# Kernel optimization log

Hardware: AMD Instinct MI355X
Metric: run time of the kernel (lower is better)

The kernel has to match this reference:

```python
import jax, jax.numpy as jnp
import numpy as np

N_QUBITS = 12
LAYERS = 8
N_CLASS = 10
BATCH = 2048
FEAT = 3072  # CIFAR-10 flattened 3*32*32
DIM = 2 ** N_QUBITS


def _apply_ry_layer(psi, angles):
    """Apply Ry(angles[q]) to qubit q for all q. psi: [B, 2,...,2] complex.
    kron order in the torch code makes qubit 0 the MSB -> tensor axis q+1."""
    c, s = jnp.cos(angles), jnp.sin(angles)
    for q in range(N_QUBITS):
        rot = jnp.stack([jnp.stack([c[q], -s[q]]), jnp.stack([s[q], c[q]])]).astype(psi.dtype)
        # contract qubit axis with rot (rows index output): psi'[..a..] = rot[a,b] psi[..b..]
        psi = jnp.moveaxis(jnp.tensordot(psi, rot, axes=([q + 1], [1])), -1, q + 1)
    return psi


def _cnot(psi, control, target):
    """CNOT == proj0(c) x I(t) + proj1(c) x X(t): flip target bit where control bit is 1."""
    ca, ta = control + 1, target + 1
    flipped = jnp.flip(psi, axis=ta)          # X on target qubit
    p0 = jax.lax.index_in_dim(psi, 0, axis=ca, keepdims=True)      # control = 0: identity
    p1 = jax.lax.index_in_dim(flipped, 1, axis=ca, keepdims=True)  # control = 1: X
    return jnp.concatenate([p0, p1], axis=ca)


def setup_inputs() -> dict:
    key = jax.random.key(0)
    kx, ka, kw = jax.random.split(key, 3)
    x = jax.random.normal(kx, (BATCH, FEAT), dtype=jnp.float32)
    angles = jax.random.uniform(ka, (LAYERS, N_QUBITS), minval=-0.01, maxval=0.01, dtype=jnp.float32)
    W = jax.random.normal(kw, (N_CLASS, DIM), dtype=jnp.float32) * np.float32(1.0 / np.sqrt(DIM))
    b = jnp.zeros((N_CLASS,), dtype=jnp.float32)
    return {"x": x, "angles": angles, "W": W, "b": b}


def reference(x, angles, W, b):
    B = x.shape[0]
    # CIFAR branch: right-pad features to 2^n, flatten (no-op for 2D), L2-normalize rows
    x = jnp.pad(x, ((0, 0), (0, DIM - x.shape[1])))
    x = x / jnp.linalg.norm(x, axis=1, keepdims=True)
    psi = x.astype(jnp.complex64).reshape((B,) + (2,) * N_QUBITS)
    for l in range(LAYERS):
        psi = _apply_ry_layer(psi, angles[l])
        # cx_linear_layer: CNOT(n-2,n-1), then CNOT(i,i+1) for i = n-3..0
        psi = _cnot(psi, N_QUBITS - 2, N_QUBITS - 1)
        for i in range(N_QUBITS - 3, -1, -1):
            psi = _cnot(psi, i, i + 1)
    probs = (psi.real ** 2 + psi.imag ** 2).reshape(B, DIM)  # Re(conj(psi)*psi)
    return probs @ W.T + b
```

## Files before the change

### kernel.cpp

```cpp
#include <hip/hip_runtime.h>
#include <math.h>

#define LAYERS  8
#define FEAT    3072
#define NCLASS  10
#define DIM     4096
#define ST      68

typedef float v2f __attribute__((ext_vector_type(2)));
typedef float v4f __attribute__((ext_vector_type(4)));

__device__ __forceinline__ int px6c(int r) {
    int u = r ^ (r >> 1); u ^= u >> 2; u ^= u >> 4; return u & 63;
}
__device__ __forceinline__ int gray6(int r) { return (r ^ (r >> 1)) & 63; }

__device__ __forceinline__ float getc(const v2f v[32], int u) {
    return (u & 1) ? v[u >> 1].y : v[u >> 1].x;
}
__device__ __forceinline__ void setc(v2f v[32], int u, float x) {
    if (u & 1) v[u >> 1].y = x; else v[u >> 1].x = x;
}
__device__ __forceinline__ float bpermf(int addr, float x) {
    return __int_as_float(__builtin_amdgcn_ds_bpermute(addr, __float_as_int(x)));
}

__device__ __forceinline__ void butterflies6(v2f v[32],
                                             const float* __restrict__ cl,
                                             const float* __restrict__ sl,
                                             int off) {
    {
        const float c = cl[off], s = sl[off];
        const v2f c2 = {c, c};
        const v2f ms = {-s, s};
#pragma unroll
        for (int i = 0; i < 32; ++i) {
            v2f a = v[i];
            v2f sw = {a.y, a.x};
            v[i] = a * c2 + sw * ms;
        }
    }
#pragma unroll
    for (int p = 1; p < 6; ++p) {
        const float c = cl[off - p], s = sl[off - p];
        const v2f c2 = {c, c};
        const v2f s2 = {s, s};
#pragma unroll
        for (int i0 = 0; i0 < 32; ++i0) {
            if (i0 & (1 << (p - 1))) continue;
            const int i1 = i0 | (1 << (p - 1));
            v2f a = v[i0], e = v[i1];
            v[i0] = a * c2 - e * s2;
            v[i1] = a * s2 + e * c2;
        }
    }
}

__device__ __forceinline__ void butterflies6_renamed(v2f v[32],
                                                     const float* __restrict__ cl,
                                                     const float* __restrict__ sl,
                                                     float psgn) {
    {
        const float c = cl[11], s = sl[11];
        const v2f c2 = {c, c};
        const v2f msA = {-s, s};
        const v2f msB = {s, -s};
#pragma unroll
        for (int k = 0; k < 32; ++k) {
            v2f a = v[k];
            v2f sw = {a.y, a.x};
            v[k] = a * c2 + sw * ((k & 1) ? msB : msA);
        }
    }
#pragma unroll
    for (int b = 1; b < 5; ++b) {
        const float c = cl[11 - b], s = sl[11 - b];
        const v2f c2 = {c, c};
#pragma unroll
        for (int m = 0; m < 32; ++m) {
            if (m & (1 << (b - 1))) continue;
            const int part = m ^ ((1 << b) - 1);
            const float sg = (m & (1 << b)) ? -s : s;
            const v2f sg2 = {sg, sg};
            const v2f A = v[m], E = v[part];
            const v2f Esw = {E.y, E.x};
            const v2f Asw = {A.y, A.x};
            v[m]    = A * c2 - Esw * sg2;
            v[part] = Asw * sg2 + E * c2;
        }
    }
    {
        const float c = cl[6];
        const float snl = psgn * sl[6];
        const v2f c2 = {c, c};
        const v2f sg2 = {snl, snl};
#pragma unroll
        for (int m = 0; m < 16; ++m) {
            const int part = m ^ 31;
            const v2f A = v[m], E = v[part];
            const v2f Esw = {E.y, E.x};
            const v2f Asw = {A.y, A.x};
            v[m]    = A * c2 - Esw * sg2;
            v[part] = Asw * sg2 + E * c2;
        }
    }
}

__global__ __launch_bounds__(64)
void qnn_kernel(const float* __restrict__ x,
                const float* __restrict__ ang,
                const float* __restrict__ W,
                const float* __restrict__ bias,
                float* __restrict__ out)
{
    __shared__ __attribute__((aligned(16))) float lds[ST * 64];
    __shared__ float cst[96], snt[96];

    const int t = threadIdx.x;
    const int b = blockIdx.x;

    {
        float a0 = ang[t];
        cst[t] = cosf(a0);
        snt[t] = sinf(a0);
        if (t < 32) {
            float a1 = ang[64 + t];
            cst[64 + t] = cosf(a1);
            snt[64 + t] = sinf(a1);
        }
    }

    v2f v[32];
    {
        const float* xb = x + (size_t)b * FEAT;
#pragma unroll
        for (int r = 0; r < 64; ++r) {
            if (r < FEAT / 64) setc(v, r, xb[64 * r + t]);
            else               setc(v, r, 0.f);
        }
    }

    float invn2;
    {
        v2f s2 = {0.f, 0.f};
#pragma unroll
        for (int i = 0; i < 32; ++i) s2 += v[i] * v[i];
        float ss = s2.x + s2.y;
#pragma unroll
        for (int o = 1; o < 64; o <<= 1) ss += __shfl_xor(ss, o, 64);
        invn2 = 1.0f / ss;
    }

    {
        const int slot = __builtin_amdgcn_s_getreg(4 | (0 << 6) | (3 << 11)) & 7;
#pragma unroll 1
        for (int i = 0; i < slot; ++i) __builtin_amdgcn_s_sleep(12);
    }

    int px = t ^ (t >> 1); px ^= px >> 2; px ^= px >> 4; px &= 63;
    const int A0 = 4 * px;
    const int A1 = 4 * (px ^ 63);
    const int u0 = t & 1;
    const float psgn = u0 ? -1.f : 1.f;
    const int gtl = gray6(t);
    const int bp  = gtl + 32 * ST * u0;
    const int bm  = gtl - 32 * ST * u0;

    {
        const float* cl = cst;
        const float* sl = snt;
        butterflies6(v, cl, sl, 5);
#pragma unroll
        for (int i = 0; i < 16; ++i) {
            v4f q = {v[2 * i].x, v[2 * i].y, v[2 * i + 1].x, v[2 * i + 1].y};
            *(v4f*)(lds + ST * t + 4 * i) = q;
        }
#pragma unroll
        for (int u = 0; u < 64; ++u)
            setc(v, u, lds[t + ST * u]);
        butterflies6(v, cl, sl, 11);
    }

#pragma unroll 1
    for (int p = 0; p < 4; ++p) {
        {
            const float* cl = cst + (2 * p + 1) * 12;
            const float* sl = snt + (2 * p + 1) * 12;

            butterflies6_renamed(v, cl, sl, psgn);

#pragma unroll
            for (int s = 0; s < 64; ++s) {
                const int g = gray6(s);
                lds[((g & 32) ? bm : bp) + ST * g] = getc(v, s);
            }
#pragma unroll
            for (int i = 0; i < 16; ++i) {
                v4f q = *(const v4f*)(lds + ST * t + 4 * i);
                v[2 * i]     = (v2f){q.x, q.y};
                v[2 * i + 1] = (v2f){q.z, q.w};
            }

            butterflies6(v, cl, sl, 5);

            if (p < 3) {
                float n[64];
#pragma unroll
                for (int r = 0; r < 64; ++r) {
                    const int srcr = px6c(r);
                    n[r] = bpermf((srcr & 1) ? A1 : A0, getc(v, srcr));
                }
#pragma unroll
                for (int r = 0; r < 64; ++r)
                    setc(v, r, n[r]);
            }
        }

        if (p == 3) break;

        {
            const float* cl = cst + (2 * p + 2) * 12;
            const float* sl = snt + (2 * p + 2) * 12;

            butterflies6(v, cl, sl, 5);
#pragma unroll
            for (int i = 0; i < 16; ++i) {
                v4f q = {v[2 * i].x, v[2 * i].y, v[2 * i + 1].x, v[2 * i + 1].y};
                *(v4f*)(lds + ST * t + 4 * i) = q;
            }
#pragma unroll
            for (int u = 0; u < 64; ++u)
                setc(v, u, lds[t + ST * u]);
            butterflies6(v, cl, sl, 11);
        }
    }

#pragma unroll
    for (int i = 0; i < 32; ++i) {
        const int g0 = 64 * gray6(2 * i);
        const int g1 = 64 * (gray6(2 * i) ^ 1);
        lds[g0 + gtl]        = v[i].x * v[i].x;
        lds[g1 + (gtl ^ 32)] = v[i].y * v[i].y;
    }

    float acc[NCLASS];
#pragma unroll
    for (int c = 0; c < NCLASS; ++c) acc[c] = 0.f;

#pragma unroll 1
    for (int k = 0; k < 16; ++k) {
        const v4f q4 = *(const v4f*)(lds + 4 * t + 256 * k);
        const float* wp = W + 4 * t + 256 * k;
#pragma unroll
        for (int c = 0; c < NCLASS; ++c) {
            const v4f w4 = *(const v4f*)(wp + c * DIM);
            acc[c] += q4.x * w4.x + q4.y * w4.y + q4.z * w4.z + q4.w * w4.w;
        }
    }

#pragma unroll
    for (int c = 0; c < NCLASS; ++c) {
        float a = acc[c];
#pragma unroll
        for (int o = 1; o < 64; o <<= 1) a += __shfl_xor(a, o, 64);
        if (t == 0) out[b * NCLASS + c] = fmaf(a, invn2, bias[c]);
    }
}

extern "C" void kernel_launch(void* const* d_in, const int* in_sizes, int n_in,
                              void* d_out, int out_size, void* d_ws, size_t ws_size,
                              hipStream_t stream) {
    const float* x    = (const float*)d_in[0];
    const float* ang  = (const float*)d_in[1];
    const float* W    = (const float*)d_in[2];
    const float* bias = (const float*)d_in[3];
    float* out = (float*)d_out;
    const int batch = in_sizes[0] / FEAT;
    qnn_kernel<<<batch, 64, 0, stream>>>(x, ang, W, bias, out);
}
```

Before: 114.9 us.

## Split each sample's state across two wavefronts with DPP intra-pair rotations

Each block now uses two 64-lane wavefronts instead of one, so each thread holds 32 amplitudes instead of 64. The qubit that pairs the two wavefronts is applied during the LDS exchange as a combined rotation, and the lane-pair qubit uses DPP quad permutes instead of register renaming. The goal is lower register pressure, higher occupancy and more latency hiding, at the cost of extra __syncthreads and a cross-wave reduction at the end. The staggered s_sleep start and the padded LDS layout are removed, and LDS addressing now uses XOR swizzles.

```diff
diff --git a/kernel.cpp b/kernel.cpp
--- a/kernel.cpp
+++ b/kernel.cpp
@@ -5,265 +5,256 @@
 #define FEAT    3072
 #define NCLASS  10
 #define DIM     4096
-#define ST      68
 
 typedef float v2f __attribute__((ext_vector_type(2)));
 typedef float v4f __attribute__((ext_vector_type(4)));
 
-__device__ __forceinline__ int px6c(int r) {
-    int u = r ^ (r >> 1); u ^= u >> 2; u ^= u >> 4; return u & 63;
-}
-__device__ __forceinline__ int gray6(int r) { return (r ^ (r >> 1)) & 63; }
-
-__device__ __forceinline__ float getc(const v2f v[32], int u) {
-    return (u & 1) ? v[u >> 1].y : v[u >> 1].x;
-}
-__device__ __forceinline__ void setc(v2f v[32], int u, float x) {
-    if (u & 1) v[u >> 1].y = x; else v[u >> 1].x = x;
-}
-__device__ __forceinline__ float bpermf(int addr, float x) {
+__device__ __forceinline__ int px6c(int r){ int u = r ^ (r>>1); u ^= u>>2; u ^= u>>4; return u & 63; }
+__device__ __forceinline__ int px5c(int r){ int u = r ^ (r>>1); u ^= u>>2; u ^= u>>4; return u & 31; }
+
+__device__ __forceinline__ float getc16(const v2f v[16], int u){ return (u&1)? v[u>>1].y : v[u>>1].x; }
+__device__ __forceinline__ void  setc16(v2f v[16], int u, float x){ if(u&1) v[u>>1].y = x; else v[u>>1].x = x; }
+
+__device__ __forceinline__ float bpermf(int addr, float x){
     return __int_as_float(__builtin_amdgcn_ds_bpermute(addr, __float_as_int(x)));
 }
-
-__device__ __forceinline__ void butterflies6(v2f v[32],
+__device__ __forceinline__ float dppx1(float x){
+    return __int_as_float(__builtin_amdgcn_update_dpp(0, __float_as_int(x), 0xB1, 0xF, 0xF, true));
+}
+
+__device__ __forceinline__ void butterflies5(v2f v[16],
                                              const float* __restrict__ cl,
                                              const float* __restrict__ sl,
-                                             int off) {
+                                             int off){
     {
         const float c = cl[off], s = sl[off];
-        const v2f c2 = {c, c};
-        const v2f ms = {-s, s};
-#pragma unroll
-        for (int i = 0; i < 32; ++i) {
-            v2f a = v[i];
-            v2f sw = {a.y, a.x};
-            v[i] = a * c2 + sw * ms;
-        }
-    }
-#pragma unroll
-    for (int p = 1; p < 6; ++p) {
-        const float c = cl[off - p], s = sl[off - p];
-        const v2f c2 = {c, c};
-        const v2f s2 = {s, s};
-#pragma unroll
-        for (int i0 = 0; i0 < 32; ++i0) {
-            if (i0 & (1 << (p - 1))) continue;
-            const int i1 = i0 | (1 << (p - 1));
-            v2f a = v[i0], e = v[i1];
-            v[i0] = a * c2 - e * s2;
-            v[i1] = a * s2 + e * c2;
-        }
-    }
-}
-
-__device__ __forceinline__ void butterflies6_renamed(v2f v[32],
-                                                     const float* __restrict__ cl,
-                                                     const float* __restrict__ sl,
-                                                     float psgn) {
-    {
-        const float c = cl[11], s = sl[11];
-        const v2f c2 = {c, c};
-        const v2f msA = {-s, s};
-        const v2f msB = {s, -s};
-#pragma unroll
-        for (int k = 0; k < 32; ++k) {
-            v2f a = v[k];
-            v2f sw = {a.y, a.x};
-            v[k] = a * c2 + sw * ((k & 1) ? msB : msA);
-        }
-    }
-#pragma unroll
-    for (int b = 1; b < 5; ++b) {
-        const float c = cl[11 - b], s = sl[11 - b];
-        const v2f c2 = {c, c};
-#pragma unroll
-        for (int m = 0; m < 32; ++m) {
-            if (m & (1 << (b - 1))) continue;
-            const int part = m ^ ((1 << b) - 1);
-            const float sg = (m & (1 << b)) ? -s : s;
-            const v2f sg2 = {sg, sg};
-            const v2f A = v[m], E = v[part];
-            const v2f Esw = {E.y, E.x};
-            const v2f Asw = {A.y, A.x};
-            v[m]    = A * c2 - Esw * sg2;
-            v[part] = Asw * sg2 + E * c2;
-        }
-    }
-    {
-        const float c = cl[6];
-        const float snl = psgn * sl[6];
-        const v2f c2 = {c, c};
-        const v2f sg2 = {snl, snl};
-#pragma unroll
-        for (int m = 0; m < 16; ++m) {
-            const int part = m ^ 31;
-            const v2f A = v[m], E = v[part];
-            const v2f Esw = {E.y, E.x};
-            const v2f Asw = {A.y, A.x};
-            v[m]    = A * c2 - Esw * sg2;
-            v[part] = Asw * sg2 + E * c2;
-        }
-    }
-}
-
-__global__ __launch_bounds__(64)
+        const v2f c2 = {c,c}, ms = {-s, s};
+#pragma unroll
+        for (int i=0;i<16;++i){ v2f a=v[i]; v2f sw={a.y,a.x}; v[i] = a*c2 + sw*ms; }
+    }
+#pragma unroll
+    for (int p=1;p<5;++p){
+        const float c = cl[off-p], s = sl[off-p];
+        const v2f c2={c,c}, s2={s,s};
+#pragma unroll
+        for (int i0=0;i0<16;++i0){
+            if (i0 & (1<<(p-1))) continue;
+            const int i1 = i0 | (1<<(p-1));
+            v2f a=v[i0], e=v[i1];
+            v[i0] = a*c2 - e*s2;
+            v[i1] = a*s2 + e*c2;
+        }
+    }
+}
+
+__global__ __launch_bounds__(128, 4)
 void qnn_kernel(const float* __restrict__ x,
                 const float* __restrict__ ang,
                 const float* __restrict__ W,
                 const float* __restrict__ bias,
                 float* __restrict__ out)
 {
-    __shared__ __attribute__((aligned(16))) float lds[ST * 64];
-    __shared__ float cst[96], snt[96];
+    __shared__ __attribute__((aligned(16))) float lds[4096];
+    __shared__ float cst[96], snt[96], nrm[2], redc[NCLASS];
 
     const int t = threadIdx.x;
+    const int w = t >> 6;
+    const int l = t & 63;
     const int b = blockIdx.x;
 
-    {
-        float a0 = ang[t];
-        cst[t] = cosf(a0);
-        snt[t] = sinf(a0);
-        if (t < 32) {
-            float a1 = ang[64 + t];
-            cst[64 + t] = cosf(a1);
-            snt[64 + t] = sinf(a1);
-        }
-    }
-
-    v2f v[32];
+    if (t < 96){ float a = ang[t]; cst[t] = cosf(a); snt[t] = sinf(a); }
+    __syncthreads();
+
+    v2f v[16];
     {
         const float* xb = x + (size_t)b * FEAT;
-#pragma unroll
-        for (int r = 0; r < 64; ++r) {
-            if (r < FEAT / 64) setc(v, r, xb[64 * r + t]);
-            else               setc(v, r, 0.f);
-        }
-    }
-
-    float invn2;
-    {
-        v2f s2 = {0.f, 0.f};
-#pragma unroll
-        for (int i = 0; i < 32; ++i) s2 += v[i] * v[i];
+        const int base = 2048*w + 32*l;
+        if (base < FEAT){
+#pragma unroll
+            for (int i=0;i<8;++i){
+                v4f q = *(const v4f*)(xb + base + 4*i);
+                v[2*i]   = (v2f){q.x, q.y};
+                v[2*i+1] = (v2f){q.z, q.w};
+            }
+        } else {
+#pragma unroll
+            for (int i=0;i<16;++i) v[i] = (v2f){0.f, 0.f};
+        }
+    }
+    {
+        v2f s2 = {0.f,0.f};
+#pragma unroll
+        for (int i=0;i<16;++i) s2 += v[i]*v[i];
         float ss = s2.x + s2.y;
 #pragma unroll
-        for (int o = 1; o < 64; o <<= 1) ss += __shfl_xor(ss, o, 64);
-        invn2 = 1.0f / ss;
-    }
-
-    {
-        const int slot = __builtin_amdgcn_s_getreg(4 | (0 << 6) | (3 << 11)) & 7;
+        for (int o=1;o<64;o<<=1) ss += __shfl_xor(ss, o, 64);
+        if (l==0) nrm[w] = ss;
+    }
+
+    const int px = px6c(l);
+    const int A0 = 4*px;
+    const int A1 = 4*(px^63);
+    const int AW = w ? A1 : A0;
+    const int wq = 2048*w;
+    int wAf[8], rBf[4], rBfw[4];
+#pragma unroll
+    for (int i=0;i<8;++i) wAf[i] = 32*l + 4*(i ^ (l&7));
+    {
+        const int l5 = l>>5;
+#pragma unroll
+        for (int g=0;g<4;++g){
+            rBf[g]  = 32*l5 + (((l&31) ^ (l5<<2)) ^ (g<<3));
+            rBfw[g] = rBf[g] + wq;
+        }
+    }
+
 #pragma unroll 1
-        for (int i = 0; i < slot; ++i) __builtin_amdgcn_s_sleep(12);
-    }
-
-    int px = t ^ (t >> 1); px ^= px >> 2; px ^= px >> 4; px &= 63;
-    const int A0 = 4 * px;
-    const int A1 = 4 * (px ^ 63);
-    const int u0 = t & 1;
-    const float psgn = u0 ? -1.f : 1.f;
-    const int gtl = gray6(t);
-    const int bp  = gtl + 32 * ST * u0;
-    const int bm  = gtl - 32 * ST * u0;
-
-    {
-        const float* cl = cst;
-        const float* sl = snt;
-        butterflies6(v, cl, sl, 5);
-#pragma unroll
-        for (int i = 0; i < 16; ++i) {
-            v4f q = {v[2 * i].x, v[2 * i].y, v[2 * i + 1].x, v[2 * i + 1].y};
-            *(v4f*)(lds + ST * t + 4 * i) = q;
-        }
-#pragma unroll
-        for (int u = 0; u < 64; ++u)
-            setc(v, u, lds[t + ST * u]);
-        butterflies6(v, cl, sl, 11);
-    }
-
+    for (int p=0;p<4;++p){
+        {
+            const float* cl = cst + 24*p;
+            const float* sl = snt + 24*p;
+            butterflies5(v, cl, sl, 11);
+            {
+                const float c = cl[6], s = sl[6];
+                const float sg = (l&1)? s : -s;
+                const v2f c2={c,c}, sg2={sg,sg};
+#pragma unroll
+                for (int k=0;k<16;++k){
+                    v2f pa = { dppx1(v[k].x), dppx1(v[k].y) };
+                    v[k] = v[k]*c2 + pa*sg2;
+                }
+            }
+            __syncthreads();
+#pragma unroll
+            for (int i=0;i<8;++i){
+                v4f q = { v[2*i].x, v[2*i].y, v[2*i+1].x, v[2*i+1].y };
+                *(v4f*)&lds[wAf[i] + wq] = q;
+            }
+            __syncthreads();
+            {
+                const float c0 = cl[0], s0 = sl[0];
+                const float ca = w ? s0 : c0;
+                const float cb = w ? c0 : -s0;
+#pragma unroll
+                for (int h=0;h<2;++h){
+                    float t0[16], t1[16];
+#pragma unroll
+                    for (int q=0;q<16;++q){
+                        const int r = 16*h + q;
+                        t0[q] = lds[rBf[r&3] + 64*r];
+                        t1[q] = lds[rBf[r&3] + 64*r + 2048];
+                    }
+#pragma unroll
+                    for (int q=0;q<16;++q)
+                        setc16(v, 16*h+q, ca*t0[q] + cb*t1[q]);
+                }
+            }
+            butterflies5(v, cl, sl, 5);
+            {
+                float n[32];
+                if (w==0){
+#pragma unroll
+                    for (int dr=0;dr<32;++dr){
+                        const int sr = px5c(dr);
+                        n[dr] = bpermf((sr&1)? A1 : A0, getc16(v, sr));
+                    }
+                } else {
+#pragma unroll
+                    for (int dr=0;dr<32;++dr){
+                        const int sr = px5c(dr) ^ 31;
+                        n[dr] = bpermf((sr&1)? A1 : A0, getc16(v, sr));
+                    }
+                }
+#pragma unroll
+                for (int dr=0;dr<32;++dr) setc16(v, dr, n[dr]);
+            }
+        }
+        {
+            const float* cl = cst + 24*p + 12;
+            const float* sl = snt + 24*p + 12;
+            butterflies5(v, cl, sl, 5);
+            __syncthreads();
+#pragma unroll
+            for (int r=0;r<32;++r) lds[rBfw[r&3] + 64*r] = getc16(v, r);
+            __syncthreads();
+            {
+                const float c0 = cl[0], s0 = sl[0];
+                const float ca = w ? s0 : c0;
+                const float cb = w ? c0 : -s0;
+#pragma unroll
+                for (int h=0;h<2;++h){
+                    float t0[16], t1[16];
+#pragma unroll
+                    for (int i=0;i<4;++i){
+                        const int ii = 4*h + i;
+                        v4f a  = *(const v4f*)&lds[wAf[ii]];
+                        v4f bq = *(const v4f*)&lds[wAf[ii] + 2048];
+                        t0[4*i]=a.x;  t0[4*i+1]=a.y;  t0[4*i+2]=a.z;  t0[4*i+3]=a.w;
+                        t1[4*i]=bq.x; t1[4*i+1]=bq.y; t1[4*i+2]=bq.z; t1[4*i+3]=bq.w;
+                    }
+#pragma unroll
+                    for (int q=0;q<16;++q)
+                        setc16(v, 16*h+q, ca*t0[q] + cb*t1[q]);
+                }
+            }
+            butterflies5(v, cl, sl, 11);
+            {
+                const float c = cl[6], s = sl[6];
+                const float sg = (l&1)? s : -s;
+                const v2f c2={c,c}, sg2={sg,sg};
+#pragma unroll
+                for (int k=0;k<16;++k){
+                    v2f pa = { dppx1(v[k].x), dppx1(v[k].y) };
+                    v[k] = v[k]*c2 + pa*sg2;
+                }
+            }
+            {
+                float ug[32], n[32];
+                const bool po = (l & 1);
+#pragma unroll
+                for (int k=0;k<32;++k) ug[k] = po ? getc16(v, k^31) : getc16(v, k);
+#pragma unroll
+                for (int dr=0;dr<32;++dr) n[dr] = bpermf(AW, ug[px5c(dr)]);
+#pragma unroll
+                for (int dr=0;dr<32;++dr) setc16(v, dr, n[dr]);
+            }
+        }
+    }
+
+    float acc[NCLASS];
+#pragma unroll
+    for (int c=0;c<NCLASS;++c) acc[c] = 0.f;
+    {
+        const float* wp0 = W + 2048*w + 32*l;
 #pragma unroll 1
-    for (int p = 0; p < 4; ++p) {
-        {
-            const float* cl = cst + (2 * p + 1) * 12;
-            const float* sl = snt + (2 * p + 1) * 12;
-
-            butterflies6_renamed(v, cl, sl, psgn);
-
-#pragma unroll
-            for (int s = 0; s < 64; ++s) {
-                const int g = gray6(s);
-                lds[((g & 32) ? bm : bp) + ST * g] = getc(v, s);
-            }
-#pragma unroll
-            for (int i = 0; i < 16; ++i) {
-                v4f q = *(const v4f*)(lds + ST * t + 4 * i);
-                v[2 * i]     = (v2f){q.x, q.y};
-                v[2 * i + 1] = (v2f){q.z, q.w};
-            }
-
-            butterflies6(v, cl, sl, 5);
-
-            if (p < 3) {
-                float n[64];
-#pragma unroll
-                for (int r = 0; r < 64; ++r) {
-                    const int srcr = px6c(r);
-                    n[r] = bpermf((srcr & 1) ? A1 : A0, getc(v, srcr));
-                }
-#pragma unroll
-                for (int r = 0; r < 64; ++r)
-                    setc(v, r, n[r]);
-            }
-        }
-
-        if (p == 3) break;
-
-        {
-            const float* cl = cst + (2 * p + 2) * 12;
-            const float* sl = snt + (2 * p + 2) * 12;
-
-            butterflies6(v, cl, sl, 5);
-#pragma unroll
-            for (int i = 0; i < 16; ++i) {
-                v4f q = {v[2 * i].x, v[2 * i].y, v[2 * i + 1].x, v[2 * i + 1].y};
-                *(v4f*)(lds + ST * t + 4 * i) = q;
-            }
-#pragma unroll
-            for (int u = 0; u < 64; ++u)
-                setc(v, u, lds[t + ST * u]);
-            butterflies6(v, cl, sl, 11);
-        }
-    }
-
-#pragma unroll
-    for (int i = 0; i < 32; ++i) {
-        const int g0 = 64 * gray6(2 * i);
-        const int g1 = 64 * (gray6(2 * i) ^ 1);
-        lds[g0 + gtl]        = v[i].x * v[i].x;
-        lds[g1 + (gtl ^ 32)] = v[i].y * v[i].y;
-    }
-
-    float acc[NCLASS];
-#pragma unroll
-    for (int c = 0; c < NCLASS; ++c) acc[c] = 0.f;
-
-#pragma unroll 1
-    for (int k = 0; k < 16; ++k) {
-        const v4f q4 = *(const v4f*)(lds + 4 * t + 256 * k);
-        const float* wp = W + 4 * t + 256 * k;
-#pragma unroll
-        for (int c = 0; c < NCLASS; ++c) {
-            const v4f w4 = *(const v4f*)(wp + c * DIM);
-            acc[c] += q4.x * w4.x + q4.y * w4.y + q4.z * w4.z + q4.w * w4.w;
-        }
-    }
-
-#pragma unroll
-    for (int c = 0; c < NCLASS; ++c) {
-        float a = acc[c];
-#pragma unroll
-        for (int o = 1; o < 64; o <<= 1) a += __shfl_xor(a, o, 64);
-        if (t == 0) out[b * NCLASS + c] = fmaf(a, invn2, bias[c]);
+        for (int k=0;k<8;++k){
+            v2f a = v[2*k], bb = v[2*k+1];
+            v4f pq = { a.x*a.x, a.y*a.y, bb.x*bb.x, bb.y*bb.y };
+            const float* wp = wp0 + 4*k;
+#pragma unroll
+            for (int c=0;c<NCLASS;++c){
+                v4f w4 = *(const v4f*)(wp + c*DIM);
+                acc[c] += pq.x*w4.x + pq.y*w4.y + pq.z*w4.z + pq.w*w4.w;
+            }
+        }
+    }
+#pragma unroll
+    for (int c=0;c<NCLASS;++c){
+        float a2 = acc[c];
+#pragma unroll
+        for (int o=1;o<64;o<<=1) a2 += __shfl_xor(a2, o, 64);
+        acc[c] = a2;
+    }
+    if (w==1 && l==0){
+#pragma unroll
+        for (int c=0;c<NCLASS;++c) redc[c] = acc[c];
+    }
+    __syncthreads();
+    if (w==0 && l==0){
+        const float invn2 = 1.f / (nrm[0] + nrm[1]);
+#pragma unroll
+        for (int c=0;c<NCLASS;++c)
+            out[b*NCLASS + c] = fmaf(acc[c] + redc[c], invn2, bias[c]);
     }
 }
 
@@ -276,5 +267,5 @@
     const float* bias = (const float*)d_in[3];
     float* out = (float*)d_out;
     const int batch = in_sizes[0] / FEAT;
-    qnn_kernel<<<batch, 64, 0, stream>>>(x, ang, W, bias, out);
-}
+    qnn_kernel<<<batch, 128, 0, stream>>>(x, ang, W, bias, out);
+}
```

New measurement: 161.1 us. 1.4x slower.

## Process two batch rows per wavefront to interleave independent work and share W loads

Applied to the files above, without the earlier changes.

Each 64-thread block now simulates two batch samples at once, holding two 64-register state vectors and using a doubled LDS buffer. The two independent streams of butterflies, LDS transposes and bpermutes can hide each other's latency, and each W load in the final projection serves both samples. The staggered-start sleep now reads a different hardware register field. The costs are roughly twice the VGPR use, likely spills or lower occupancy, and half as many blocks.

```diff
diff --git a/kernel.cpp b/kernel.cpp
--- a/kernel.cpp
+++ b/kernel.cpp
@@ -6,6 +6,7 @@
 #define NCLASS  10
 #define DIM     4096
 #define ST      68
+#define SBF     (ST * 64)
 
 typedef float v2f __attribute__((ext_vector_type(2)));
 typedef float v4f __attribute__((ext_vector_type(4)));
@@ -106,18 +107,21 @@
     }
 }
 
-__global__ __launch_bounds__(64)
+__global__ __launch_bounds__(64, 1)
 void qnn_kernel(const float* __restrict__ x,
                 const float* __restrict__ ang,
                 const float* __restrict__ W,
                 const float* __restrict__ bias,
-                float* __restrict__ out)
+                float* __restrict__ out,
+                int batch)
 {
-    __shared__ __attribute__((aligned(16))) float lds[ST * 64];
+    __shared__ __attribute__((aligned(16))) float lds[2 * SBF];
     __shared__ float cst[96], snt[96];
 
     const int t = threadIdx.x;
     const int b = blockIdx.x;
+    const int b0 = 2 * b, b1 = 2 * b + 1;
+    const bool has1 = (b1 < batch);
 
     {
         float a0 = ang[t];
@@ -130,29 +134,49 @@
         }
     }
 
-    v2f v[32];
-    {
-        const float* xb = x + (size_t)b * FEAT;
+    v2f v0[32], v1[32];
+    {
+        const float* xb = x + (size_t)b0 * FEAT;
 #pragma unroll
         for (int r = 0; r < 64; ++r) {
-            if (r < FEAT / 64) setc(v, r, xb[64 * r + t]);
-            else               setc(v, r, 0.f);
-        }
-    }
-
-    float invn2;
+            if (r < FEAT / 64) setc(v0, r, xb[64 * r + t]);
+            else               setc(v0, r, 0.f);
+        }
+    }
+    if (has1) {
+        const float* xb = x + (size_t)b1 * FEAT;
+#pragma unroll
+        for (int r = 0; r < 64; ++r) {
+            if (r < FEAT / 64) setc(v1, r, xb[64 * r + t]);
+            else               setc(v1, r, 0.f);
+        }
+    } else {
+#pragma unroll
+        for (int i = 0; i < 32; ++i) v1[i] = (v2f){0.f, 0.f};
+    }
+
+    float invn0, invn1;
     {
         v2f s2 = {0.f, 0.f};
 #pragma unroll
-        for (int i = 0; i < 32; ++i) s2 += v[i] * v[i];
+        for (int i = 0; i < 32; ++i) s2 += v0[i] * v0[i];
         float ss = s2.x + s2.y;
 #pragma unroll
         for (int o = 1; o < 64; o <<= 1) ss += __shfl_xor(ss, o, 64);
-        invn2 = 1.0f / ss;
-    }
-
-    {
-        const int slot = __builtin_amdgcn_s_getreg(4 | (0 << 6) | (3 << 11)) & 7;
+        invn0 = 1.0f / ss;
+    }
+    {
+        v2f s2 = {0.f, 0.f};
+#pragma unroll
+        for (int i = 0; i < 32; ++i) s2 += v1[i] * v1[i];
+        float ss = s2.x + s2.y;
+#pragma unroll
+        for (int o = 1; o < 64; o <<= 1) ss += __shfl_xor(ss, o, 64);
+        invn1 = 1.0f / ss;
+    }
+
+    {
+        const int slot = __builtin_amdgcn_s_getreg(4 | (4 << 6) | (1 << 11)) & 3;
 #pragma unroll 1
         for (int i = 0; i < slot; ++i) __builtin_amdgcn_s_sleep(12);
     }
@@ -166,19 +190,53 @@
     const int bp  = gtl + 32 * ST * u0;
     const int bm  = gtl - 32 * ST * u0;
 
+    auto storeRows = [&](const v2f* vv, const int SB) {
+#pragma unroll
+        for (int i = 0; i < 16; ++i) {
+            v4f q = {vv[2 * i].x, vv[2 * i].y, vv[2 * i + 1].x, vv[2 * i + 1].y};
+            *(v4f*)(lds + SB + ST * t + 4 * i) = q;
+        }
+    };
+    auto readCols = [&](v2f* vv, const int SB) {
+#pragma unroll
+        for (int u = 0; u < 64; ++u)
+            setc(vv, u, lds[SB + t + ST * u]);
+    };
+    auto foldedStore = [&](const v2f* vv, const int SB) {
+#pragma unroll
+        for (int s = 0; s < 64; ++s) {
+            const int g = gray6(s);
+            lds[SB + ((g & 32) ? bm : bp) + ST * g] = getc(vv, s);
+        }
+    };
+    auto rowRead = [&](v2f* vv, const int SB) {
+#pragma unroll
+        for (int i = 0; i < 16; ++i) {
+            v4f q = *(const v4f*)(lds + SB + ST * t + 4 * i);
+            vv[2 * i]     = (v2f){q.x, q.y};
+            vv[2 * i + 1] = (v2f){q.z, q.w};
+        }
+    };
+    auto grayB = [&](v2f* vv) {
+        float n[64];
+#pragma unroll
+        for (int r = 0; r < 64; ++r) {
+            const int srcr = px6c(r);
+            n[r] = bpermf((srcr & 1) ? A1 : A0, getc(vv, srcr));
+        }
+#pragma unroll
+        for (int r = 0; r < 64; ++r) setc(vv, r, n[r]);
+    };
+
     {
         const float* cl = cst;
         const float* sl = snt;
-        butterflies6(v, cl, sl, 5);
-#pragma unroll
-        for (int i = 0; i < 16; ++i) {
-            v4f q = {v[2 * i].x, v[2 * i].y, v[2 * i + 1].x, v[2 * i + 1].y};
-            *(v4f*)(lds + ST * t + 4 * i) = q;
-        }
-#pragma unroll
-        for (int u = 0; u < 64; ++u)
-            setc(v, u, lds[t + ST * u]);
-        butterflies6(v, cl, sl, 11);
+        butterflies6(v0, cl, sl, 5);
+        butterflies6(v1, cl, sl, 5);
+        storeRows(v0, 0);  storeRows(v1, SBF);
+        readCols(v0, 0);   readCols(v1, SBF);
+        butterflies6(v0, cl, sl, 11);
+        butterflies6(v1, cl, sl, 11);
     }
 
 #pragma unroll 1
@@ -187,32 +245,16 @@
             const float* cl = cst + (2 * p + 1) * 12;
             const float* sl = snt + (2 * p + 1) * 12;
 
-            butterflies6_renamed(v, cl, sl, psgn);
-
-#pragma unroll
-            for (int s = 0; s < 64; ++s) {
-                const int g = gray6(s);
-                lds[((g & 32) ? bm : bp) + ST * g] = getc(v, s);
-            }
-#pragma unroll
-            for (int i = 0; i < 16; ++i) {
-                v4f q = *(const v4f*)(lds + ST * t + 4 * i);
-                v[2 * i]     = (v2f){q.x, q.y};
-                v[2 * i + 1] = (v2f){q.z, q.w};
-            }
-
-            butterflies6(v, cl, sl, 5);
+            butterflies6_renamed(v0, cl, sl, psgn);
+            butterflies6_renamed(v1, cl, sl, psgn);
+            foldedStore(v0, 0);  foldedStore(v1, SBF);
+            rowRead(v0, 0);      rowRead(v1, SBF);
+            butterflies6(v0, cl, sl, 5);
+            butterflies6(v1, cl, sl, 5);
 
             if (p < 3) {
-                float n[64];
-#pragma unroll
-                for (int r = 0; r < 64; ++r) {
-                    const int srcr = px6c(r);
-                    n[r] = bpermf((srcr & 1) ? A1 : A0, getc(v, srcr));
-                }
-#pragma unroll
-                for (int r = 0; r < 64; ++r)
-                    setc(v, r, n[r]);
+                grayB(v0);
+                grayB(v1);
             }
         }
 
@@ -222,16 +264,12 @@
             const float* cl = cst + (2 * p + 2) * 12;
             const float* sl = snt + (2 * p + 2) * 12;
 
-            butterflies6(v, cl, sl, 5);
-#pragma unroll
-            for (int i = 0; i < 16; ++i) {
-                v4f q = {v[2 * i].x, v[2 * i].y, v[2 * i + 1].x, v[2 * i + 1].y};
-                *(v4f*)(lds + ST * t + 4 * i) = q;
-            }
-#pragma unroll
-            for (int u = 0; u < 64; ++u)
-                setc(v, u, lds[t + ST * u]);
-            butterflies6(v, cl, sl, 11);
+            butterflies6(v0, cl, sl, 5);
+            butterflies6(v1, cl, sl, 5);
+            storeRows(v0, 0);  storeRows(v1, SBF);
+            readCols(v0, 0);   readCols(v1, SBF);
+            butterflies6(v0, cl, sl, 11);
+            butterflies6(v1, cl, sl, 11);
         }
     }
 
@@ -239,31 +277,41 @@
     for (int i = 0; i < 32; ++i) {
         const int g0 = 64 * gray6(2 * i);
         const int g1 = 64 * (gray6(2 * i) ^ 1);
-        lds[g0 + gtl]        = v[i].x * v[i].x;
-        lds[g1 + (gtl ^ 32)] = v[i].y * v[i].y;
-    }
-
-    float acc[NCLASS];
-#pragma unroll
-    for (int c = 0; c < NCLASS; ++c) acc[c] = 0.f;
+        lds[g0 + gtl]        = v0[i].x * v0[i].x;
+        lds[g1 + (gtl ^ 32)] = v0[i].y * v0[i].y;
+        lds[SBF + g0 + gtl]        = v1[i].x * v1[i].x;
+        lds[SBF + g1 + (gtl ^ 32)] = v1[i].y * v1[i].y;
+    }
+
+    float acc0[NCLASS], acc1[NCLASS];
+#pragma unroll
+    for (int c = 0; c < NCLASS; ++c) { acc0[c] = 0.f; acc1[c] = 0.f; }
 
 #pragma unroll 1
     for (int k = 0; k < 16; ++k) {
-        const v4f q4 = *(const v4f*)(lds + 4 * t + 256 * k);
+        const v4f qa = *(const v4f*)(lds + 4 * t + 256 * k);
+        const v4f qb = *(const v4f*)(lds + SBF + 4 * t + 256 * k);
         const float* wp = W + 4 * t + 256 * k;
 #pragma unroll
         for (int c = 0; c < NCLASS; ++c) {
             const v4f w4 = *(const v4f*)(wp + c * DIM);
-            acc[c] += q4.x * w4.x + q4.y * w4.y + q4.z * w4.z + q4.w * w4.w;
+            acc0[c] += qa.x * w4.x + qa.y * w4.y + qa.z * w4.z + qa.w * w4.w;
+            acc1[c] += qb.x * w4.x + qb.y * w4.y + qb.z * w4.z + qb.w * w4.w;
         }
     }
 
 #pragma unroll
     for (int c = 0; c < NCLASS; ++c) {
-        float a = acc[c];
-#pragma unroll
-        for (int o = 1; o < 64; o <<= 1) a += __shfl_xor(a, o, 64);
-        if (t == 0) out[b * NCLASS + c] = fmaf(a, invn2, bias[c]);
+        float a0 = acc0[c], a1 = acc1[c];
+#pragma unroll
+        for (int o = 1; o < 64; o <<= 1) {
+            a0 += __shfl_xor(a0, o, 64);
+            a1 += __shfl_xor(a1, o, 64);
+        }
+        if (t == 0) {
+            out[b0 * NCLASS + c] = fmaf(a0, invn0, bias[c]);
+            if (has1) out[b1 * NCLASS + c] = fmaf(a1, invn1, bias[c]);
+        }
     }
 }
 
@@ -276,5 +324,6 @@
     const float* bias = (const float*)d_in[3];
     float* out = (float*)d_out;
     const int batch = in_sizes[0] / FEAT;
-    qnn_kernel<<<batch, 64, 0, stream>>>(x, ang, W, bias, out);
-}
+    const int blocks = (batch + 1) / 2;
+    qnn_kernel<<<blocks, 64, 0, stream>>>(x, ang, W, bias, out, batch);
+}
```

After: 122.2 us. 6.4% more time.
